# Optimization experiments

Hardware: AMD Instinct MI355X
Metric: run time of the kernel (lower is better)

Reference implementation:

```python
import jax, jax.numpy as jnp
import numpy as np

B = 16384            # number of subgraphs in the batch
NODES_PER_G = 50     # nodes per subgraph
N = B * NODES_PER_G  # total nodes = 819200
L = 3                # num_gcn_layers
EMB = 32             # emb_dim -> repr dim = (1+L)*EMB = 128
REPR = (1 + L) * EMB
PFEAT, FEAT = 1280, 200
P, D, I = 2000, 10000, 20000
RELS = 2


def setup_inputs() -> dict:
    key = jax.random.key(0)
    ks = jax.random.split(key, 16)
    node_repr = jax.random.normal(ks[0], (N, REPR), jnp.float32)
    profeat = jax.random.normal(ks[1], (P, PFEAT), jnp.float32)
    drugfeat = jax.random.normal(ks[2], (D, FEAT), jnp.float32)
    s1p = 1.0 / np.sqrt(PFEAT); s2 = 1.0 / np.sqrt(EMB); s1 = 1.0 / np.sqrt(FEAT)
    W1p = jax.random.normal(ks[3], (PFEAT, EMB), jnp.float32) * s1p
    b1p = jnp.zeros((EMB,), jnp.float32)
    W2p = jax.random.normal(ks[4], (EMB, EMB), jnp.float32) * s2
    b2p = jnp.zeros((EMB,), jnp.float32)
    W1 = jax.random.normal(ks[5], (FEAT, EMB), jnp.float32) * s1
    b1 = jnp.zeros((EMB,), jnp.float32)
    W2 = jax.random.normal(ks[6], (EMB, EMB), jnp.float32) * s2
    b2 = jnp.zeros((EMB,), jnp.float32)
    fc_in = 3 * REPR + 2 * EMB  # 448
    fc_W = jax.random.normal(ks[7], (fc_in, RELS), jnp.float32) / np.sqrt(fc_in)
    fc_b = jnp.zeros((RELS,), jnp.float32)
    # batched-graph structure: contiguous blocks of NODES_PER_G nodes per graph
    graph_ids = (jnp.arange(N, dtype=jnp.int32) // NODES_PER_G).astype(jnp.int32)
    # exactly one head (id==1) and one tail (id==2) node per graph -> their indices
    head_ids = (jnp.arange(B, dtype=jnp.int32) * NODES_PER_G)
    tail_ids = head_ids + 1
    node_idx = jax.random.randint(ks[8], (N,), 0, I, jnp.int32)
    proind = jax.random.randint(ks[9], (I,), 0, P, jnp.int32)
    drugind = jax.random.randint(ks[10], (I,), 0, D, jnp.int32)
    return dict(node_repr=node_repr, profeat=profeat, drugfeat=drugfeat,
                W1p=W1p, b1p=b1p, W2p=W2p, b2p=b2p,
                W1=W1, b1=b1, W2=W2, b2=b2, fc_W=fc_W, fc_b=fc_b,
                graph_ids=graph_ids, head_ids=head_ids, tail_ids=tail_ids,
                node_idx=node_idx, proind=proind, drugind=drugind)


def reference(node_repr, profeat, drugfeat, W1p, b1p, W2p, b2p,
              W1, b1, W2, b2, fc_W, fc_b,
              graph_ids, head_ids, tail_ids, node_idx, proind, drugind):
    # mean_nodes(g, 'repr'): per-graph mean pooling of node reprs
    sums = jax.ops.segment_sum(node_repr, graph_ids, num_segments=B)      # [B, REPR]
    cnts = jax.ops.segment_sum(jnp.ones((node_repr.shape[0],), node_repr.dtype),
                               graph_ids, num_segments=B)                # [B]
    g_out = sums / cnts[:, None]
    # head/tail embedding gathers (id==1 / id==2 nodes)
    head_embs = node_repr[head_ids]                                       # [B, REPR]
    tail_embs = node_repr[tail_ids]                                       # [B, REPR]
    # nested table lookups: profeat[proind[idx[head]]], drugfeat[drugind[idx[tail]]]
    head_feat = profeat[proind[node_idx[head_ids]]]                       # [B, PFEAT]
    tail_feat = drugfeat[drugind[node_idx[tail_ids]]]                     # [B, FEAT]
    # small fuse MLPs (dropout is identity in eval)
    fuse1 = jax.nn.relu(head_feat @ W1p + b1p) @ W2p + b2p                # [B, EMB]
    fuse2 = jax.nn.relu(tail_feat @ W1 + b1) @ W2 + b2                    # [B, EMB]
    g_rep = jnp.concatenate([g_out, head_embs, tail_embs, fuse1, fuse2], axis=1)
    return g_rep @ fc_W + fc_b                                            # [B, RELS]
```

## Files before the change

kernel.cpp:

```cpp
#include <hip/hip_runtime.h>
#include <hip/hip_bf16.h>

#define B_GRAPHS 16384
#define NODES_PER_G 50
#define REPR 128
#define PFEAT 1280
#define FEAT 200
#define EMB 32
#define P_ROWS 2000
#define D_ROWS 10000


__global__ __launch_bounds__(256) void fuse_all_kernel(
    const float* __restrict__ profeat,
    const float* __restrict__ drugfeat,
    const float* __restrict__ W1p,
    const float* __restrict__ b1p,
    const float* __restrict__ W2p,
    const float* __restrict__ W1,
    const float* __restrict__ b1,
    const float* __restrict__ W2,
    const float* __restrict__ fcW,
    float*       __restrict__ f1out,
    float*       __restrict__ f2out)
{
    const int grp  = threadIdx.x >> 5;
    const int lane = threadIdx.x & 31;
    const int bid  = blockIdx.x;

    if (bid < P_ROWS / 8) {
        const int p = bid * 8 + grp;
        float m0 = 0.f, m1 = 0.f;
        #pragma unroll
        for (int k = 0; k < 32; ++k) {
            float w = W2p[lane * 32 + k];
            float2 fw = *(const float2*)(fcW + (384 + k) * 2);
            m0 = fmaf(w, fw.x, m0);
            m1 = fmaf(w, fw.y, m1);
        }
        const float4* pf4 = (const float4*)(profeat + (long)p * PFEAT);
        float a0 = 0.f, a1 = 0.f, a2 = 0.f, a3 = 0.f;
        #pragma unroll 4
        for (int q = 0; q < PFEAT / 4; q += 4) {
            float4 f0 = pf4[q], f1 = pf4[q + 1], f2 = pf4[q + 2], f3 = pf4[q + 3];
            int k = q * 4;
            a0 = fmaf(f0.x, W1p[(k + 0) * 32 + lane], a0);
            a0 = fmaf(f0.y, W1p[(k + 1) * 32 + lane], a0);
            a0 = fmaf(f0.z, W1p[(k + 2) * 32 + lane], a0);
            a0 = fmaf(f0.w, W1p[(k + 3) * 32 + lane], a0);
            a1 = fmaf(f1.x, W1p[(k + 4) * 32 + lane], a1);
            a1 = fmaf(f1.y, W1p[(k + 5) * 32 + lane], a1);
            a1 = fmaf(f1.z, W1p[(k + 6) * 32 + lane], a1);
            a1 = fmaf(f1.w, W1p[(k + 7) * 32 + lane], a1);
            a2 = fmaf(f2.x, W1p[(k + 8) * 32 + lane], a2);
            a2 = fmaf(f2.y, W1p[(k + 9) * 32 + lane], a2);
            a2 = fmaf(f2.z, W1p[(k + 10) * 32 + lane], a2);
            a2 = fmaf(f2.w, W1p[(k + 11) * 32 + lane], a2);
            a3 = fmaf(f3.x, W1p[(k + 12) * 32 + lane], a3);
            a3 = fmaf(f3.y, W1p[(k + 13) * 32 + lane], a3);
            a3 = fmaf(f3.z, W1p[(k + 14) * 32 + lane], a3);
            a3 = fmaf(f3.w, W1p[(k + 15) * 32 + lane], a3);
        }
        float h = fmaxf((a0 + a1) + (a2 + a3) + b1p[lane], 0.f);
        float p0 = h * m0, p1 = h * m1;
        for (int m = 16; m >= 1; m >>= 1) {
            p0 += __shfl_xor(p0, m, 32);
            p1 += __shfl_xor(p1, m, 32);
        }
        if (lane == 0) {
            f1out[p * 2 + 0] = p0;
            f1out[p * 2 + 1] = p1;
        }
    } else {
        const int d = (bid - P_ROWS / 8) * 8 + grp;
        float m0 = 0.f, m1 = 0.f;
        #pragma unroll
        for (int k = 0; k < 32; ++k) {
            float w = W2[lane * 32 + k];
            float2 fw = *(const float2*)(fcW + (416 + k) * 2);
            m0 = fmaf(w, fw.x, m0);
            m1 = fmaf(w, fw.y, m1);
        }
        const float4* df4 = (const float4*)(drugfeat + (long)d * FEAT);
        float a0 = 0.f, a1 = 0.f;
        #pragma unroll 5
        for (int q = 0; q < FEAT / 4; q += 2) {
            float4 f0 = df4[q], f1 = df4[q + 1];
            int k = q * 4;
            a0 = fmaf(f0.x, W1[(k + 0) * 32 + lane], a0);
            a0 = fmaf(f0.y, W1[(k + 1) * 32 + lane], a0);
            a0 = fmaf(f0.z, W1[(k + 2) * 32 + lane], a0);
            a0 = fmaf(f0.w, W1[(k + 3) * 32 + lane], a0);
            a1 = fmaf(f1.x, W1[(k + 4) * 32 + lane], a1);
            a1 = fmaf(f1.y, W1[(k + 5) * 32 + lane], a1);
            a1 = fmaf(f1.z, W1[(k + 6) * 32 + lane], a1);
            a1 = fmaf(f1.w, W1[(k + 7) * 32 + lane], a1);
        }
        float h = fmaxf(a0 + a1 + b1[lane], 0.f);
        float p0 = h * m0, p1 = h * m1;
        for (int m = 16; m >= 1; m >>= 1) {
            p0 += __shfl_xor(p0, m, 32);
            p1 += __shfl_xor(p1, m, 32);
        }
        if (lane == 0) {
            f2out[d * 2 + 0] = p0;
            f2out[d * 2 + 1] = p1;
        }
    }
}

__global__ __launch_bounds__(256) void main_kernel(
    const float* __restrict__ nr,
    const float* __restrict__ fcW,
    const float* __restrict__ fcb,
    const float* __restrict__ b2p,
    const float* __restrict__ b2,
    const int*   __restrict__ head_ids,
    const int*   __restrict__ tail_ids,
    const int*   __restrict__ node_idx,
    const int*   __restrict__ proind,
    const int*   __restrict__ drugind,
    const float* __restrict__ f1out,
    const float* __restrict__ f2out,
    float*       __restrict__ out)
{
    const int g    = blockIdx.x * 8 + (threadIdx.x >> 5);
    const int lane = threadIdx.x & 31;

    const int hnode = head_ids[g];
    const int tnode = tail_ids[g];
    const int prow  = proind[node_idx[hnode]];
    const int drow  = drugind[node_idx[tnode]];
    const float2 f1v = *(const float2*)(f1out + prow * 2);
    const float2 f2v = *(const float2*)(f2out + drow * 2);

    const float4* nr4 = (const float4*)nr;
    const long base4 = (long)g * (NODES_PER_G * REPR / 4);

    float4 head4 = nr4[base4 + 0 * 32 + lane];
    float4 tail4 = nr4[base4 + 1 * 32 + lane];
    float4 s0, s1;
    s0.x = s0.y = s0.z = s0.w = 0.f;
    s1.x = s1.y = s1.z = s1.w = 0.f;
    #pragma unroll 8
    for (int i = 2; i < NODES_PER_G; i += 2) {
        float4 fa = nr4[base4 + i * 32 + lane];
        float4 fb = nr4[base4 + (i + 1) * 32 + lane];
        s0.x += fa.x; s0.y += fa.y; s0.z += fa.z; s0.w += fa.w;
        s1.x += fb.x; s1.y += fb.y; s1.z += fb.z; s1.w += fb.w;
    }
    float4 pool;
    pool.x = head4.x + tail4.x + s0.x + s1.x;
    pool.y = head4.y + tail4.y + s0.y + s1.y;
    pool.z = head4.z + tail4.z + s0.z + s1.z;
    pool.w = head4.w + tail4.w + s0.w + s1.w;

    const float4* fcW4 = (const float4*)fcW;
    float4 wg0 = fcW4[lane * 2 + 0],       wg1 = fcW4[lane * 2 + 1];
    float4 wh0 = fcW4[64 + lane * 2 + 0],  wh1 = fcW4[64 + lane * 2 + 1];
    float4 wt0 = fcW4[128 + lane * 2 + 0], wt1 = fcW4[128 + lane * 2 + 1];

    const float inv50 = 1.0f / (float)NODES_PER_G;
    float p0 = inv50 * (pool.x * wg0.x + pool.y * wg0.z + pool.z * wg1.x + pool.w * wg1.z)
             + head4.x * wh0.x + head4.y * wh0.z + head4.z * wh1.x + head4.w * wh1.z
             + tail4.x * wt0.x + tail4.y * wt0.z + tail4.z * wt1.x + tail4.w * wt1.z;
    float p1 = inv50 * (pool.x * wg0.y + pool.y * wg0.w + pool.z * wg1.y + pool.w * wg1.w)
             + head4.x * wh0.y + head4.y * wh0.w + head4.z * wh1.y + head4.w * wh1.w
             + tail4.x * wt0.y + tail4.y * wt0.w + tail4.z * wt1.y + tail4.w * wt1.w;

    {
        float2 fw1 = *(const float2*)(fcW + (384 + lane) * 2);
        float2 fw2 = *(const float2*)(fcW + (416 + lane) * 2);
        float bb1 = b2p[lane], bb2 = b2[lane];
        p0 = fmaf(bb1, fw1.x, fmaf(bb2, fw2.x, p0));
        p1 = fmaf(bb1, fw1.y, fmaf(bb2, fw2.y, p1));
    }

    for (int m = 16; m >= 1; m >>= 1) {
        p0 += __shfl_xor(p0, m, 32);
        p1 += __shfl_xor(p1, m, 32);
    }
    if (lane == 0) {
        out[g * 2 + 0] = p0 + f1v.x + f2v.x + fcb[0];
        out[g * 2 + 1] = p1 + f1v.y + f2v.y + fcb[1];
    }
}

extern "C" void kernel_launch(void* const* d_in, const int* in_sizes, int n_in,
                              void* d_out, int out_size, void* d_ws, size_t ws_size,
                              hipStream_t stream) {
    const float* node_repr = (const float*)d_in[0];
    const float* profeat   = (const float*)d_in[1];
    const float* drugfeat  = (const float*)d_in[2];
    const float* W1p       = (const float*)d_in[3];
    const float* b1p       = (const float*)d_in[4];
    const float* W2p       = (const float*)d_in[5];
    const float* b2p       = (const float*)d_in[6];
    const float* W1        = (const float*)d_in[7];
    const float* b1        = (const float*)d_in[8];
    const float* W2        = (const float*)d_in[9];
    const float* b2        = (const float*)d_in[10];
    const float* fc_W      = (const float*)d_in[11];
    const float* fc_b      = (const float*)d_in[12];
    const int* head_ids    = (const int*)d_in[14];
    const int* tail_ids    = (const int*)d_in[15];
    const int* node_idx    = (const int*)d_in[16];
    const int* proind      = (const int*)d_in[17];
    const int* drugind     = (const int*)d_in[18];

    float* f1out = (float*)d_ws;
    float* f2out = (float*)d_ws + 2 * P_ROWS;
    float* out   = (float*)d_out;

    hipLaunchKernelGGL(fuse_all_kernel, dim3(P_ROWS / 8 + D_ROWS / 8), dim3(256), 0, stream,
                       profeat, drugfeat, W1p, b1p, W2p, W1, b1, W2, fc_W,
                       f1out, f2out);

    hipLaunchKernelGGL(main_kernel, dim3(B_GRAPHS / 8), dim3(256), 0, stream,
                       node_repr, fc_W, fc_b, b2p, b2,
                       head_ids, tail_ids, node_idx, proind, drugind,
                       f1out, f2out, out);
}
```

Before: 120.5 us.

## Run fuse-MLP and pooling in one launch, add small finalize kernel

Merges the per-row fuse MLP precompute and the per-graph pooling/FC pass into a single kernel with block ranges, so the bandwidth-heavy node_repr streaming no longer waits behind the fuse precompute. The dependent gather of f1/f2 and the bias add move to a lightweight finalize kernel that reads back and rewrites the output. The cost is an extra launch and a read-modify-write of the output, but the two large phases can now overlap.

```diff
diff --git a/kernel.cpp b/kernel.cpp
--- a/kernel.cpp
+++ b/kernel.cpp
@@ -10,8 +10,14 @@
 #define P_ROWS 2000
 #define D_ROWS 10000
 
-
-__global__ __launch_bounds__(256) void fuse_all_kernel(
+#define NPF (P_ROWS / 8)
+#define NDF (D_ROWS / 8)
+#define NFUSE (NPF + NDF)
+#define NPOOL (B_GRAPHS / 8)
+
+
+__global__ __launch_bounds__(256) void merged_kernel(
+    const float* __restrict__ nr,
     const float* __restrict__ profeat,
     const float* __restrict__ drugfeat,
     const float* __restrict__ W1p,
@@ -21,14 +27,17 @@
     const float* __restrict__ b1,
     const float* __restrict__ W2,
     const float* __restrict__ fcW,
+    const float* __restrict__ b2p,
+    const float* __restrict__ b2,
     float*       __restrict__ f1out,
-    float*       __restrict__ f2out)
+    float*       __restrict__ f2out,
+    float*       __restrict__ out)
 {
     const int grp  = threadIdx.x >> 5;
     const int lane = threadIdx.x & 31;
     const int bid  = blockIdx.x;
 
-    if (bid < P_ROWS / 8) {
+    if (bid < NPF) {
         const int p = bid * 8 + grp;
         float m0 = 0.f, m1 = 0.f;
         #pragma unroll
@@ -71,8 +80,8 @@
             f1out[p * 2 + 0] = p0;
             f1out[p * 2 + 1] = p1;
         }
-    } else {
-        const int d = (bid - P_ROWS / 8) * 8 + grp;
+    } else if (bid < NFUSE) {
+        const int d = (bid - NPF) * 8 + grp;
         float m0 = 0.f, m1 = 0.f;
         #pragma unroll
         for (int k = 0; k < 32; ++k) {
@@ -106,15 +115,62 @@
             f2out[d * 2 + 0] = p0;
             f2out[d * 2 + 1] = p1;
         }
+    } else {
+        const int g = (bid - NFUSE) * 8 + grp;
+        const float4* nr4 = (const float4*)nr;
+        const long base4 = (long)g * (NODES_PER_G * REPR / 4);
+
+        float4 head4 = nr4[base4 + 0 * 32 + lane];
+        float4 tail4 = nr4[base4 + 1 * 32 + lane];
+        float4 s0, s1;
+        s0.x = s0.y = s0.z = s0.w = 0.f;
+        s1.x = s1.y = s1.z = s1.w = 0.f;
+        #pragma unroll 8
+        for (int i = 2; i < NODES_PER_G; i += 2) {
+            float4 fa = nr4[base4 + i * 32 + lane];
+            float4 fb = nr4[base4 + (i + 1) * 32 + lane];
+            s0.x += fa.x; s0.y += fa.y; s0.z += fa.z; s0.w += fa.w;
+            s1.x += fb.x; s1.y += fb.y; s1.z += fb.z; s1.w += fb.w;
+        }
+        float4 pool;
+        pool.x = head4.x + tail4.x + s0.x + s1.x;
+        pool.y = head4.y + tail4.y + s0.y + s1.y;
+        pool.z = head4.z + tail4.z + s0.z + s1.z;
+        pool.w = head4.w + tail4.w + s0.w + s1.w;
+
+        const float4* fcW4 = (const float4*)fcW;
+        float4 wg0 = fcW4[lane * 2 + 0],       wg1 = fcW4[lane * 2 + 1];
+        float4 wh0 = fcW4[64 + lane * 2 + 0],  wh1 = fcW4[64 + lane * 2 + 1];
+        float4 wt0 = fcW4[128 + lane * 2 + 0], wt1 = fcW4[128 + lane * 2 + 1];
+
+        const float inv50 = 1.0f / (float)NODES_PER_G;
+        float p0 = inv50 * (pool.x * wg0.x + pool.y * wg0.z + pool.z * wg1.x + pool.w * wg1.z)
+                 + head4.x * wh0.x + head4.y * wh0.z + head4.z * wh1.x + head4.w * wh1.z
+                 + tail4.x * wt0.x + tail4.y * wt0.z + tail4.z * wt1.x + tail4.w * wt1.z;
+        float p1 = inv50 * (pool.x * wg0.y + pool.y * wg0.w + pool.z * wg1.y + pool.w * wg1.w)
+                 + head4.x * wh0.y + head4.y * wh0.w + head4.z * wh1.y + head4.w * wh1.w
+                 + tail4.x * wt0.y + tail4.y * wt0.w + tail4.z * wt1.y + tail4.w * wt1.w;
+
+        {
+            float2 fw1 = *(const float2*)(fcW + (384 + lane) * 2);
+            float2 fw2 = *(const float2*)(fcW + (416 + lane) * 2);
+            float bb1 = b2p[lane], bb2 = b2[lane];
+            p0 = fmaf(bb1, fw1.x, fmaf(bb2, fw2.x, p0));
+            p1 = fmaf(bb1, fw1.y, fmaf(bb2, fw2.y, p1));
+        }
+
+        for (int m = 16; m >= 1; m >>= 1) {
+            p0 += __shfl_xor(p0, m, 32);
+            p1 += __shfl_xor(p1, m, 32);
+        }
+        if (lane == 0) {
+            out[g * 2 + 0] = p0;
+            out[g * 2 + 1] = p1;
+        }
     }
 }
 
-__global__ __launch_bounds__(256) void main_kernel(
-    const float* __restrict__ nr,
-    const float* __restrict__ fcW,
-    const float* __restrict__ fcb,
-    const float* __restrict__ b2p,
-    const float* __restrict__ b2,
+__global__ __launch_bounds__(256) void finalize_kernel(
     const int*   __restrict__ head_ids,
     const int*   __restrict__ tail_ids,
     const int*   __restrict__ node_idx,
@@ -122,68 +178,19 @@
     const int*   __restrict__ drugind,
     const float* __restrict__ f1out,
     const float* __restrict__ f2out,
+    const float* __restrict__ fcb,
     float*       __restrict__ out)
 {
-    const int g    = blockIdx.x * 8 + (threadIdx.x >> 5);
-    const int lane = threadIdx.x & 31;
-
-    const int hnode = head_ids[g];
-    const int tnode = tail_ids[g];
-    const int prow  = proind[node_idx[hnode]];
-    const int drow  = drugind[node_idx[tnode]];
+    const int g = blockIdx.x * 256 + threadIdx.x;
+    if (g >= B_GRAPHS) return;
+    const int prow = proind[node_idx[head_ids[g]]];
+    const int drow = drugind[node_idx[tail_ids[g]]];
     const float2 f1v = *(const float2*)(f1out + prow * 2);
     const float2 f2v = *(const float2*)(f2out + drow * 2);
-
-    const float4* nr4 = (const float4*)nr;
-    const long base4 = (long)g * (NODES_PER_G * REPR / 4);
-
-    float4 head4 = nr4[base4 + 0 * 32 + lane];
-    float4 tail4 = nr4[base4 + 1 * 32 + lane];
-    float4 s0, s1;
-    s0.x = s0.y = s0.z = s0.w = 0.f;
-    s1.x = s1.y = s1.z = s1.w = 0.f;
-    #pragma unroll 8
-    for (int i = 2; i < NODES_PER_G; i += 2) {
-        float4 fa = nr4[base4 + i * 32 + lane];
-        float4 fb = nr4[base4 + (i + 1) * 32 + lane];
-        s0.x += fa.x; s0.y += fa.y; s0.z += fa.z; s0.w += fa.w;
-        s1.x += fb.x; s1.y += fb.y; s1.z += fb.z; s1.w += fb.w;
-    }
-    float4 pool;
-    pool.x = head4.x + tail4.x + s0.x + s1.x;
-    pool.y = head4.y + tail4.y + s0.y + s1.y;
-    pool.z = head4.z + tail4.z + s0.z + s1.z;
-    pool.w = head4.w + tail4.w + s0.w + s1.w;
-
-    const float4* fcW4 = (const float4*)fcW;
-    float4 wg0 = fcW4[lane * 2 + 0],       wg1 = fcW4[lane * 2 + 1];
-    float4 wh0 = fcW4[64 + lane * 2 + 0],  wh1 = fcW4[64 + lane * 2 + 1];
-    float4 wt0 = fcW4[128 + lane * 2 + 0], wt1 = fcW4[128 + lane * 2 + 1];
-
-    const float inv50 = 1.0f / (float)NODES_PER_G;
-    float p0 = inv50 * (pool.x * wg0.x + pool.y * wg0.z + pool.z * wg1.x + pool.w * wg1.z)
-             + head4.x * wh0.x + head4.y * wh0.z + head4.z * wh1.x + head4.w * wh1.z
-             + tail4.x * wt0.x + tail4.y * wt0.z + tail4.z * wt1.x + tail4.w * wt1.z;
-    float p1 = inv50 * (pool.x * wg0.y + pool.y * wg0.w + pool.z * wg1.y + pool.w * wg1.w)
-             + head4.x * wh0.y + head4.y * wh0.w + head4.z * wh1.y + head4.w * wh1.w
-             + tail4.x * wt0.y + tail4.y * wt0.w + tail4.z * wt1.y + tail4.w * wt1.w;
-
-    {
-        float2 fw1 = *(const float2*)(fcW + (384 + lane) * 2);
-        float2 fw2 = *(const float2*)(fcW + (416 + lane) * 2);
-        float bb1 = b2p[lane], bb2 = b2[lane];
-        p0 = fmaf(bb1, fw1.x, fmaf(bb2, fw2.x, p0));
-        p1 = fmaf(bb1, fw1.y, fmaf(bb2, fw2.y, p1));
-    }
-
-    for (int m = 16; m >= 1; m >>= 1) {
-        p0 += __shfl_xor(p0, m, 32);
-        p1 += __shfl_xor(p1, m, 32);
-    }
-    if (lane == 0) {
-        out[g * 2 + 0] = p0 + f1v.x + f2v.x + fcb[0];
-        out[g * 2 + 1] = p1 + f1v.y + f2v.y + fcb[1];
-    }
+    float2 o = *(float2*)(out + g * 2);
+    o.x += f1v.x + f2v.x + fcb[0];
+    o.y += f1v.y + f2v.y + fcb[1];
+    *(float2*)(out + g * 2) = o;
 }
 
 extern "C" void kernel_launch(void* const* d_in, const int* in_sizes, int n_in,
@@ -212,12 +219,11 @@
     float* f2out = (float*)d_ws + 2 * P_ROWS;
     float* out   = (float*)d_out;
 
-    hipLaunchKernelGGL(fuse_all_kernel, dim3(P_ROWS / 8 + D_ROWS / 8), dim3(256), 0, stream,
-                       profeat, drugfeat, W1p, b1p, W2p, W1, b1, W2, fc_W,
-                       f1out, f2out);
-
-    hipLaunchKernelGGL(main_kernel, dim3(B_GRAPHS / 8), dim3(256), 0, stream,
-                       node_repr, fc_W, fc_b, b2p, b2,
+    hipLaunchKernelGGL(merged_kernel, dim3(NFUSE + NPOOL), dim3(256), 0, stream,
+                       node_repr, profeat, drugfeat, W1p, b1p, W2p, W1, b1, W2,
+                       fc_W, b2p, b2, f1out, f2out, out);
+
+    hipLaunchKernelGGL(finalize_kernel, dim3(B_GRAPHS / 256), dim3(256), 0, stream,
                        head_ids, tail_ids, node_idx, proind, drugind,
-                       f1out, f2out, out);
+                       f1out, f2out, fc_b, out);
 }
```

After: 110.7 us. 1.09x faster.
